# Optimization experiments

Hardware: AMD Instinct MI355X
Metric: run time of the kernel (lower is better)

The kernel has to match this reference:

```python
import jax, jax.numpy as jnp
import numpy as np

D_MODEL = 1024
NUM_HEADS = 16
HEAD_DIM = D_MODEL // NUM_HEADS
THETA = 10000.0


def _rope(x):
    # x: [B, H, S, Dk]; interleaved even/odd rotation as in the torch module
    *_, seq_len, d_k = x.shape
    d = d_k // 2
    inv_freq = 1.0 / (THETA ** (2.0 * jnp.arange(d, dtype=jnp.float32) / d_k))
    pos = jnp.arange(seq_len, dtype=jnp.float32)
    angles = pos[:, None] * inv_freq[None, :]  # [S, d]
    cos = jnp.cos(angles)
    sin = jnp.sin(angles)
    x_even = x[..., 0::2]
    x_odd = x[..., 1::2]
    rot_even = x_even * cos - x_odd * sin
    rot_odd = x_even * sin + x_odd * cos
    return jnp.stack([rot_even, rot_odd], axis=-1).reshape(x.shape)


def setup_inputs() -> dict:
    key = jax.random.key(0)
    ks = jax.random.split(key, 5)
    B, S = 4, 2048
    x = jax.random.normal(ks[0], (B, S, D_MODEL), dtype=jnp.float32)
    q_w = jax.random.uniform(ks[1], (D_MODEL, D_MODEL), dtype=jnp.float32)
    k_w = jax.random.uniform(ks[2], (D_MODEL, D_MODEL), dtype=jnp.float32)
    v_w = jax.random.uniform(ks[3], (D_MODEL, D_MODEL), dtype=jnp.float32)
    o_w = jax.random.uniform(ks[4], (D_MODEL, D_MODEL), dtype=jnp.float32)
    return {"x": x, "q_w": q_w, "k_w": k_w, "v_w": v_w, "o_w": o_w}


def reference(x, q_w, k_w, v_w, o_w):
    B, S, _ = x.shape
    def split_heads(t):
        return t.reshape(B, S, NUM_HEADS, HEAD_DIM).transpose(0, 2, 1, 3)  # [B,H,S,Dk]
    Q = split_heads(x @ q_w.T)
    K = split_heads(x @ k_w.T)
    V = split_heads(x @ v_w.T)
    Q = _rope(Q)
    K = _rope(K)
    scale = 1.0 / jnp.sqrt(jnp.float32(HEAD_DIM))
    scores = jnp.einsum('bhqd,bhkd->bhqk', Q, K) * scale  # [B,H,S,S]
    causal = jnp.tril(jnp.ones((S, S), dtype=bool))
    scores = jnp.where(causal[None, None], scores, -jnp.inf)
    attn = jax.nn.softmax(scores, axis=-1)
    out = jnp.einsum('bhqk,bhkd->bhqd', attn, V)  # [B,H,S,Dk]
    out = out.transpose(0, 2, 1, 3).reshape(B, S, D_MODEL)
    return out @ o_w.T
```

## Files before the change

### kernel.cpp

```cpp
#include <hip/hip_runtime.h>
#include <hip/hip_bf16.h>
#include <cstdint>
#include <cstddef>

#define D_MODEL   1024
#define NUM_HEADS 16
#define HEAD_DIM  64
#define SEQ       2048
#define BATCH     4
#define BH        (BATCH*NUM_HEADS)
#define MROWS     (BATCH*SEQ)

typedef _Float16 half8  __attribute__((ext_vector_type(8)));
typedef _Float16 half4v __attribute__((ext_vector_type(4)));
typedef float    floatx4 __attribute__((ext_vector_type(4)));

__device__ inline void gld_lds16(const void* g, void* l) {
    __builtin_amdgcn_global_load_lds(
        (__attribute__((address_space(1))) void*)g,
        (__attribute__((address_space(3))) void*)l,
        16, 0, 0);
}

__global__ void rope_table(float2* __restrict__ tab) {
    const int i = blockIdx.x * blockDim.x + threadIdx.x;
    const int p = i & 31, s = i >> 5;
    const double inv = pow(10000.0, -(double)p / 32.0);
    const double ang = (double)s * inv;
    tab[i] = make_float2((float)cos(ang), (float)sin(ang));
}

__global__ void f32_split_f16(const float* __restrict__ in,
                              _Float16* __restrict__ hi,
                              _Float16* __restrict__ lo, int n4) {
    int i = blockIdx.x * blockDim.x + threadIdx.x;
    if (i >= n4) return;
    float4 v = ((const float4*)in)[i];
    half4v h = { (_Float16)v.x, (_Float16)v.y, (_Float16)v.z, (_Float16)v.w };
    half4v l = { (_Float16)(v.x - (float)h.x), (_Float16)(v.y - (float)h.y),
                 (_Float16)(v.z - (float)h.z), (_Float16)(v.w - (float)h.w) };
    ((half4v*)hi)[i] = h;
    ((half4v*)lo)[i] = l;
}

__global__ void conv_weights(const float* __restrict__ qw, const float* __restrict__ kw,
                             const float* __restrict__ vw, const float* __restrict__ ow,
                             _Float16* __restrict__ qwh, _Float16* __restrict__ qwl,
                             _Float16* __restrict__ kwh, _Float16* __restrict__ kwl,
                             _Float16* __restrict__ vwh, _Float16* __restrict__ owh) {
    const int i = blockIdx.x * blockDim.x + threadIdx.x;
    const int which = i >> 18;
    const int j = i & 262143;
    const float4 v = ((const float4*)(which == 0 ? qw : which == 1 ? kw :
                                      which == 2 ? vw : ow))[j];
    half4v h = { (_Float16)v.x, (_Float16)v.y, (_Float16)v.z, (_Float16)v.w };
    if (which < 2) {
        half4v l = { (_Float16)(v.x - (float)h.x), (_Float16)(v.y - (float)h.y),
                     (_Float16)(v.z - (float)h.z), (_Float16)(v.w - (float)h.w) };
        ((half4v*)(which ? kwh : qwh))[j] = h;
        ((half4v*)(which ? kwl : qwl))[j] = l;
    } else {
        ((half4v*)(which == 2 ? vwh : owh))[j] = h;
    }
}

__global__ __launch_bounds__(256)
void gemm_bt(const _Float16* __restrict__ A, const _Float16* __restrict__ B,
             float* __restrict__ Cout, int M, int N, int K) {
    __shared__ _Float16 As[128*32];
    __shared__ _Float16 Bs[128*32];

    const int nb = N >> 7;
    const int bx = blockIdx.x % nb;
    const int by = blockIdx.x / nb;
    const int m0 = by << 7, n0 = bx << 7;

    const int t    = threadIdx.x;
    const int w    = t >> 6;
    const int lane = t & 63;
    const int r    = lane & 15;
    const int quad = lane >> 4;
    const int wm   = (w >> 1) << 6;
    const int wn   = (w & 1) << 6;

    const int srow = lane >> 2;
    const int scol = (lane & 3) << 3;

    floatx4 acc[4][4];
    #pragma unroll
    for (int i = 0; i < 4; i++)
        #pragma unroll
        for (int j = 0; j < 4; j++)
            acc[i][j] = (floatx4){0.f, 0.f, 0.f, 0.f};

    for (int k0 = 0; k0 < K; k0 += 32) {
        __syncthreads();
        #pragma unroll
        for (int p = 0; p < 2; ++p) {
            const int rbase = p*64 + w*16;
            gld_lds16(&A[(size_t)(m0 + rbase + srow)*K + k0 + scol], &As[rbase*32]);
            gld_lds16(&B[(size_t)(n0 + rbase + srow)*K + k0 + scol], &Bs[rbase*32]);
        }
        __syncthreads();

        half8 af[4], bf[4];
        #pragma unroll
        for (int i = 0; i < 4; i++)
            af[i] = *(const half8*)&As[(wm + i*16 + r)*32 + quad*8];
        #pragma unroll
        for (int j = 0; j < 4; j++)
            bf[j] = *(const half8*)&Bs[(wn + j*16 + r)*32 + quad*8];

        #pragma unroll
        for (int i = 0; i < 4; i++)
            #pragma unroll
            for (int j = 0; j < 4; j++)
                acc[i][j] = __builtin_amdgcn_mfma_f32_16x16x32_f16(
                                af[i], bf[j], acc[i][j], 0, 0, 0);
    }

    #pragma unroll
    for (int i = 0; i < 4; i++)
        #pragma unroll
        for (int j = 0; j < 4; j++)
            #pragma unroll
            for (int v = 0; v < 4; v++) {
                const int m = m0 + wm + i*16 + quad*4 + v;
                const int n = n0 + wn + j*16 + r;
                Cout[(size_t)m*N + n] = acc[i][j][v];
            }
}

__global__ __launch_bounds__(256)
void gemm_qkv(const _Float16* __restrict__ Axh, const _Float16* __restrict__ Axl,
              const _Float16* __restrict__ qwh, const _Float16* __restrict__ qwl,
              const _Float16* __restrict__ kwh, const _Float16* __restrict__ kwl,
              const _Float16* __restrict__ vwh,
              _Float16* __restrict__ Qhi, _Float16* __restrict__ Qlo,
              _Float16* __restrict__ Khi, _Float16* __restrict__ Klo,
              _Float16* __restrict__ Vt,  const float2* __restrict__ tab) {
    __shared__ _Float16 smem[4*4096];
    _Float16* Ash = smem;
    _Float16* Asl = smem + 4096;
    _Float16* Bsh = smem + 8192;
    _Float16* Bsl = smem + 12288;

    const int bxa = blockIdx.x;
    const int bx  = bxa % 24;
    const int by  = bxa / 24;
    const int wt  = bx >> 3;
    const int n0  = (bx & 7) << 7;
    const int m0  = by << 7;

    const _Float16* Bh = (wt == 0) ? qwh : (wt == 1) ? kwh : vwh;
    const _Float16* Bl = (wt == 0) ? qwl : kwl;

    const int t    = threadIdx.x;
    const int w    = t >> 6;
    const int lane = t & 63;
    const int r    = lane & 15;
    const int quad = lane >> 4;
    const int wm   = (w >> 1) << 6;
    const int wn   = (w & 1) << 6;

    const int srow = lane >> 2;
    const int scol = (lane & 3) << 3;

    floatx4 acc[4][4];
    #pragma unroll
    for (int i = 0; i < 4; i++)
        #pragma unroll
        for (int j = 0; j < 4; j++)
            acc[i][j] = (floatx4){0.f, 0.f, 0.f, 0.f};

    for (int k0 = 0; k0 < 1024; k0 += 32) {
        __syncthreads();
        #pragma unroll
        for (int p = 0; p < 2; ++p) {
            const int rbase = p*64 + w*16;
            const size_t ga = (size_t)(m0 + rbase + srow)*1024 + k0 + scol;
            const size_t gb = (size_t)(n0 + rbase + srow)*1024 + k0 + scol;
            gld_lds16(&Axh[ga], &Ash[rbase*32]);
            gld_lds16(&Bh [gb], &Bsh[rbase*32]);
            if (wt < 2) {
                gld_lds16(&Axl[ga], &Asl[rbase*32]);
                gld_lds16(&Bl [gb], &Bsl[rbase*32]);
            }
        }
        __syncthreads();

        half8 ah[4], bh[4];
        #pragma unroll
        for (int i = 0; i < 4; i++)
            ah[i] = *(const half8*)&Ash[(wm + i*16 + r)*32 + quad*8];
        #pragma unroll
        for (int j = 0; j < 4; j++)
            bh[j] = *(const half8*)&Bsh[(wn + j*16 + r)*32 + quad*8];

        if (wt < 2) {
            half8 al[4], bl[4];
            #pragma unroll
            for (int i = 0; i < 4; i++)
                al[i] = *(const half8*)&Asl[(wm + i*16 + r)*32 + quad*8];
            #pragma unroll
            for (int j = 0; j < 4; j++)
                bl[j] = *(const half8*)&Bsl[(wn + j*16 + r)*32 + quad*8];
            #pragma unroll
            for (int i = 0; i < 4; i++)
                #pragma unroll
                for (int j = 0; j < 4; j++) {
                    acc[i][j] = __builtin_amdgcn_mfma_f32_16x16x32_f16(
                                    ah[i], bh[j], acc[i][j], 0, 0, 0);
                    acc[i][j] = __builtin_amdgcn_mfma_f32_16x16x32_f16(
                                    ah[i], bl[j], acc[i][j], 0, 0, 0);
                    acc[i][j] = __builtin_amdgcn_mfma_f32_16x16x32_f16(
                                    al[i], bh[j], acc[i][j], 0, 0, 0);
                }
        } else {
            #pragma unroll
            for (int i = 0; i < 4; i++)
                #pragma unroll
                for (int j = 0; j < 4; j++)
                    acc[i][j] = __builtin_amdgcn_mfma_f32_16x16x32_f16(
                                    ah[i], bh[j], acc[i][j], 0, 0, 0);
        }
    }

    __syncthreads();
    float* sc = (float*)smem + w*1088;
    const int g  = lane & 7;
    const int rw = lane >> 3;
    const int hh = (n0 + wn) >> 6;

    if (wt < 2) {
        _Float16* Chi = wt ? Khi : Qhi;
        _Float16* Clo = wt ? Klo : Qlo;
        #pragma unroll
        for (int i = 0; i < 4; i++) {
            #pragma unroll
            for (int j = 0; j < 4; j++)
                #pragma unroll
                for (int v = 0; v < 4; v++)
                    sc[(quad*4 + v)*68 + j*16 + r] = acc[i][j][v];
            #pragma unroll
            for (int rg = 0; rg < 2; rg++) {
                const int row = rw + rg*8;
                const int m   = m0 + wm + i*16 + row;
                const int bb  = m >> 11, s_ = m & 2047;
                const float4 va = *(const float4*)&sc[row*68 + g*8];
                const float4 vb = *(const float4*)&sc[row*68 + g*8 + 4];
                const float vv[8] = {va.x, va.y, va.z, va.w,
                                     vb.x, vb.y, vb.z, vb.w};
                half8 hv, lv;
                #pragma unroll
                for (int p2 = 0; p2 < 4; p2++) {
                    const float2 cs = tab[s_*32 + g*4 + p2];
                    const float e0 = vv[2*p2], o0 = vv[2*p2+1];
                    const float re = e0*cs.x - o0*cs.y;
                    const float ro = e0*cs.y + o0*cs.x;
                    const _Float16 rh = (_Float16)re;
                    const _Float16 oh = (_Float16)ro;
                    hv[2*p2]   = rh; lv[2*p2]   = (_Float16)(re - (float)rh);
                    hv[2*p2+1] = oh; lv[2*p2+1] = (_Float16)(ro - (float)oh);
                }
                const size_t idx = ((((size_t)bb*NUM_HEADS + hh)*SEQ + s_) << 6) + g*8;
                *(half8*)&Chi[idx] = hv;
                *(half8*)&Clo[idx] = lv;
            }
        }
    } else {
        const int d = lane;
        #pragma unroll
        for (int i = 0; i < 4; i++) {
            #pragma unroll
            for (int j = 0; j < 4; j++)
                #pragma unroll
                for (int v = 0; v < 4; v++)
                    sc[(quad*4 + v)*68 + j*16 + r] = acc[i][j][v];
            #pragma unroll
            for (int rg = 0; rg < 2; rg++) {
                const int m  = m0 + wm + i*16 + rg*8;
                const int bb = m >> 11, s_ = m & 2047;
                half8 ov;
                #pragma unroll
                for (int rr = 0; rr < 8; rr++)
                    ov[rr] = (_Float16)sc[(rg*8 + rr)*68 + d];
                *(half8*)&Vt[((((size_t)bb*NUM_HEADS + hh)*HEAD_DIM + d) << 11) + s_] = ov;
            }
        }
    }
}

#define PSTR 72
__global__ __launch_bounds__(256)
void flash_attn(const _Float16* __restrict__ Qhi, const _Float16* __restrict__ Qlo,
                const _Float16* __restrict__ Khi, const _Float16* __restrict__ Klo,
                const _Float16* __restrict__ Vt,  _Float16* __restrict__ AO) {
    __shared__ _Float16 SB[2][6][64*32];
    __shared__ _Float16 Pl[4][16*PSTR];

    const int t    = threadIdx.x;
    const int w    = t >> 6;
    const int lane = t & 63;
    const int r    = lane & 15;
    const int quad = lane >> 4;

    const int bx = blockIdx.x;
    const int bh = bx & 63;
    const int qb = 31 - (bx >> 6);
    const int q0w = qb*64 + w*16;
    const int b  = bh >> 4, h = bh & 15;

    const _Float16* Qh_ = Qhi + (size_t)bh * SEQ * HEAD_DIM;
    const _Float16* Ql_ = Qlo + (size_t)bh * SEQ * HEAD_DIM;
    const _Float16* Khg = Khi + (size_t)bh * SEQ * HEAD_DIM;
    const _Float16* Klg = Klo + (size_t)bh * SEQ * HEAD_DIM;
    const _Float16* Vtg = Vt  + (size_t)bh * HEAD_DIM * SEQ;

    half8 qh[2], ql[2];
    #pragma unroll
    for (int c = 0; c < 2; ++c) {
        qh[c] = *(const half8*)&Qh_[(size_t)(q0w + r)*64 + c*32 + quad*8];
        ql[c] = *(const half8*)&Ql_[(size_t)(q0w + r)*64 + c*32 + quad*8];
    }

    floatx4 ot[4];
    #pragma unroll
    for (int dt = 0; dt < 4; ++dt) ot[dt] = (floatx4){0.f,0.f,0.f,0.f};
    float mi = -1e30f, li = 0.f;

    const int sr = lane >> 2;
    const int sc = (lane & 3) << 3;
    const int rb = w << 4;

    auto stage = [&](int buf, int kt) {
        const int k0  = kt << 6;
        const int row = rb + sr;
        const size_t kr = (size_t)(k0 + row)*64;
        gld_lds16(&Khg[kr +      sc], &SB[buf][0][rb*32]);
        gld_lds16(&Khg[kr + 32 + sc], &SB[buf][1][rb*32]);
        gld_lds16(&Klg[kr +      sc], &SB[buf][2][rb*32]);
        gld_lds16(&Klg[kr + 32 + sc], &SB[buf][3][rb*32]);
        const size_t vr = (size_t)row*SEQ + k0;
        gld_lds16(&Vtg[vr +      sc], &SB[buf][4][rb*32]);
        gld_lds16(&Vtg[vr + 32 + sc], &SB[buf][5][rb*32]);
    };

    const int niter = qb + 1;
    stage(0, 0);
    int cur = 0;

    for (int kt = 0; kt < niter; ++kt) {
        const int k0 = kt << 6;

        __syncthreads();
        if (kt + 1 < niter) stage(cur ^ 1, kt + 1);

        const _Float16* Kh0 = SB[cur][0];
        const _Float16* Kh1 = SB[cur][1];
        const _Float16* Kl0 = SB[cur][2];
        const _Float16* Kl1 = SB[cur][3];
        const _Float16* Vp0 = SB[cur][4];
        const _Float16* Vp1 = SB[cur][5];

        float s[16];
        __builtin_amdgcn_s_setprio(1);
        #pragma unroll
        for (int sub = 0; sub < 4; ++sub) {
            floatx4 a = (floatx4){0.f,0.f,0.f,0.f};
            const int fr = (sub*16 + r)*32 + quad*8;
            const half8 kh0 = *(const half8*)&Kh0[fr];
            const half8 kh1 = *(const half8*)&Kh1[fr];
            const half8 kl0 = *(const half8*)&Kl0[fr];
            const half8 kl1 = *(const half8*)&Kl1[fr];
            a = __builtin_amdgcn_mfma_f32_16x16x32_f16(kh0, qh[0], a, 0, 0, 0);
            a = __builtin_amdgcn_mfma_f32_16x16x32_f16(kh1, qh[1], a, 0, 0, 0);
            a = __builtin_amdgcn_mfma_f32_16x16x32_f16(kh0, ql[0], a, 0, 0, 0);
            a = __builtin_amdgcn_mfma_f32_16x16x32_f16(kh1, ql[1], a, 0, 0, 0);
            a = __builtin_amdgcn_mfma_f32_16x16x32_f16(kl0, qh[0], a, 0, 0, 0);
            a = __builtin_amdgcn_mfma_f32_16x16x32_f16(kl1, qh[1], a, 0, 0, 0);
            #pragma unroll
            for (int v = 0; v < 4; ++v) s[sub*4 + v] = a[v] * 0.125f;
        }
        __builtin_amdgcn_s_setprio(0);

        if (kt == niter - 1) {
            #pragma unroll
            for (int sub = 0; sub < 4; ++sub)
                #pragma unroll
                for (int v = 0; v < 4; ++v)
                    if (k0 + sub*16 + quad*4 + v > q0w + r)
                        s[sub*4 + v] = -1e30f;
        }

        float tm = s[0];
        #pragma unroll
        for (int i = 1; i < 16; ++i) tm = fmaxf(tm, s[i]);
        tm = fmaxf(tm, __shfl_xor(tm, 16));
        tm = fmaxf(tm, __shfl_xor(tm, 32));
        const float mn = fmaxf(mi, tm);
        const float alpha = __expf(mi - mn);
        mi = mn;
        float rs = 0.f;
        #pragma unroll
        for (int i = 0; i < 16; ++i) { s[i] = __expf(s[i] - mn); rs += s[i]; }
        rs += __shfl_xor(rs, 16);
        rs += __shfl_xor(rs, 32);
        li = li*alpha + rs;
        #pragma unroll
        for (int dt = 0; dt < 4; ++dt)
            #pragma unroll
            for (int v = 0; v < 4; ++v) ot[dt][v] *= alpha;

        #pragma unroll
        for (int sub = 0; sub < 4; ++sub) {
            half4v pk = { (_Float16)s[sub*4+0], (_Float16)s[sub*4+1],
                          (_Float16)s[sub*4+2], (_Float16)s[sub*4+3] };
            *(half4v*)&Pl[w][r*PSTR + sub*16 + quad*4] = pk;
        }

        __builtin_amdgcn_s_setprio(1);
        #pragma unroll
        for (int c = 0; c < 2; ++c) {
            const half8 pf = *(const half8*)&Pl[w][r*PSTR + c*32 + quad*8];
            const _Float16* Vsc = c ? Vp1 : Vp0;
            #pragma unroll
            for (int dt = 0; dt < 4; ++dt) {
                const half8 vf = *(const half8*)&Vsc[(dt*16 + r)*32 + quad*8];
                ot[dt] = __builtin_amdgcn_mfma_f32_16x16x32_f16(vf, pf, ot[dt], 0, 0, 0);
            }
        }
        __builtin_amdgcn_s_setprio(0);

        cur ^= 1;
    }

    const float inv = 1.0f / li;
    const int q = q0w + r;
    #pragma unroll
    for (int dt = 0; dt < 4; ++dt) {
        half4v o = { (_Float16)(ot[dt][0]*inv), (_Float16)(ot[dt][1]*inv),
                     (_Float16)(ot[dt][2]*inv), (_Float16)(ot[dt][3]*inv) };
        *(half4v*)&AO[((size_t)(b*SEQ + q))*D_MODEL + h*HEAD_DIM + dt*16 + quad*4] = o;
    }
}

extern "C" void kernel_launch(void* const* d_in, const int* in_sizes, int n_in,
                              void* d_out, int out_size, void* d_ws, size_t ws_size,
                              hipStream_t stream) {
    const float* x  = (const float*)d_in[0];
    const float* qw = (const float*)d_in[1];
    const float* kw = (const float*)d_in[2];
    const float* vw = (const float*)d_in[3];
    const float* ow = (const float*)d_in[4];
    float* out = (float*)d_out;

    _Float16* xh  = (_Float16*)d_ws;
    _Float16* xl  = xh  + (size_t)MROWS * D_MODEL;
    _Float16* qwh = xl  + (size_t)MROWS * D_MODEL;
    _Float16* qwl = qwh + (size_t)D_MODEL * D_MODEL;
    _Float16* kwh = qwl + (size_t)D_MODEL * D_MODEL;
    _Float16* kwl = kwh + (size_t)D_MODEL * D_MODEL;
    _Float16* vwh = kwl + (size_t)D_MODEL * D_MODEL;
    _Float16* owh = vwh + (size_t)D_MODEL * D_MODEL;
    _Float16* Qhi = owh + (size_t)D_MODEL * D_MODEL;
    _Float16* Qlo = Qhi + (size_t)MROWS * D_MODEL;
    _Float16* Khi = Qlo + (size_t)MROWS * D_MODEL;
    _Float16* Klo = Khi + (size_t)MROWS * D_MODEL;
    _Float16* Vt  = Klo + (size_t)MROWS * D_MODEL;
    _Float16* AO  = Vt  + (size_t)MROWS * D_MODEL;
    float2*   tab = (float2*)(AO + (size_t)MROWS * D_MODEL);

    rope_table<<<(SEQ*32)/256, 256, 0, stream>>>(tab);

    const int nx4 = MROWS * D_MODEL / 4;
    f32_split_f16<<<nx4/256, 256, 0, stream>>>(x, xh, xl, nx4);
    conv_weights<<<(4*262144)/256, 256, 0, stream>>>(qw, kw, vw, ow,
                                                     qwh, qwl, kwh, kwl, vwh, owh);

    gemm_qkv<<<64*24, 256, 0, stream>>>(xh, xl, qwh, qwl, kwh, kwl, vwh,
                                        Qhi, Qlo, Khi, Klo, Vt, tab);

    flash_attn<<<BH * (SEQ/64), 256, 0, stream>>>(Qhi, Qlo, Khi, Klo, Vt, AO);

    gemm_bt<<<(MROWS/128)*(D_MODEL/128), 256, 0, stream>>>(AO, owh, out,
                                                           MROWS, D_MODEL, D_MODEL);
}
```

Measured before the change: 389.3 us.

## Process two 64-row query groups per flash-attention block to reuse K/V tiles

Each flash-attention block now covers 128 query rows, split into two 64-row groups, instead of 64. Every wave keeps two independent online-softmax states and applies each staged K/V tile to both groups, which halves the number of K/V tile loads per query row. The price is more registers, half as many blocks (1024), and a longer critical path per block.

```diff
diff --git a/kernel.cpp b/kernel.cpp
--- a/kernel.cpp
+++ b/kernel.cpp
@@ -307,8 +307,10 @@
 
     const int bx = blockIdx.x;
     const int bh = bx & 63;
-    const int qb = 31 - (bx >> 6);
-    const int q0w = qb*64 + w*16;
+    const int qb = 15 - (bx >> 6);
+    const int Q0 = qb << 7;
+    const int q0a = Q0 + w*16;
+    const int q0b = Q0 + 64 + w*16;
     const int b  = bh >> 4, h = bh & 15;
 
     const _Float16* Qh_ = Qhi + (size_t)bh * SEQ * HEAD_DIM;
@@ -317,17 +319,22 @@
     const _Float16* Klg = Klo + (size_t)bh * SEQ * HEAD_DIM;
     const _Float16* Vtg = Vt  + (size_t)bh * HEAD_DIM * SEQ;
 
-    half8 qh[2], ql[2];
+    half8 qh0[2], ql0[2], qh1[2], ql1[2];
     #pragma unroll
     for (int c = 0; c < 2; ++c) {
-        qh[c] = *(const half8*)&Qh_[(size_t)(q0w + r)*64 + c*32 + quad*8];
-        ql[c] = *(const half8*)&Ql_[(size_t)(q0w + r)*64 + c*32 + quad*8];
-    }
-
-    floatx4 ot[4];
+        qh0[c] = *(const half8*)&Qh_[(size_t)(q0a + r)*64 + c*32 + quad*8];
+        ql0[c] = *(const half8*)&Ql_[(size_t)(q0a + r)*64 + c*32 + quad*8];
+        qh1[c] = *(const half8*)&Qh_[(size_t)(q0b + r)*64 + c*32 + quad*8];
+        ql1[c] = *(const half8*)&Ql_[(size_t)(q0b + r)*64 + c*32 + quad*8];
+    }
+
+    floatx4 ot0[4], ot1[4];
     #pragma unroll
-    for (int dt = 0; dt < 4; ++dt) ot[dt] = (floatx4){0.f,0.f,0.f,0.f};
-    float mi = -1e30f, li = 0.f;
+    for (int dt = 0; dt < 4; ++dt) {
+        ot0[dt] = (floatx4){0.f,0.f,0.f,0.f};
+        ot1[dt] = (floatx4){0.f,0.f,0.f,0.f};
+    }
+    float mi0 = -1e30f, li0 = 0.f, mi1 = -1e30f, li1 = 0.f;
 
     const int sr = lane >> 2;
     const int sc = (lane & 3) << 3;
@@ -346,7 +353,7 @@
         gld_lds16(&Vtg[vr + 32 + sc], &SB[buf][5][rb*32]);
     };
 
-    const int niter = qb + 1;
+    const int niter = 2*qb + 2;
     stage(0, 0);
     int cur = 0;
 
@@ -363,85 +370,103 @@
         const _Float16* Vp0 = SB[cur][4];
         const _Float16* Vp1 = SB[cur][5];
 
-        float s[16];
-        __builtin_amdgcn_s_setprio(1);
-        #pragma unroll
-        for (int sub = 0; sub < 4; ++sub) {
-            floatx4 a = (floatx4){0.f,0.f,0.f,0.f};
-            const int fr = (sub*16 + r)*32 + quad*8;
-            const half8 kh0 = *(const half8*)&Kh0[fr];
-            const half8 kh1 = *(const half8*)&Kh1[fr];
-            const half8 kl0 = *(const half8*)&Kl0[fr];
-            const half8 kl1 = *(const half8*)&Kl1[fr];
-            a = __builtin_amdgcn_mfma_f32_16x16x32_f16(kh0, qh[0], a, 0, 0, 0);
-            a = __builtin_amdgcn_mfma_f32_16x16x32_f16(kh1, qh[1], a, 0, 0, 0);
-            a = __builtin_amdgcn_mfma_f32_16x16x32_f16(kh0, ql[0], a, 0, 0, 0);
-            a = __builtin_amdgcn_mfma_f32_16x16x32_f16(kh1, ql[1], a, 0, 0, 0);
-            a = __builtin_amdgcn_mfma_f32_16x16x32_f16(kl0, qh[0], a, 0, 0, 0);
-            a = __builtin_amdgcn_mfma_f32_16x16x32_f16(kl1, qh[1], a, 0, 0, 0);
-            #pragma unroll
-            for (int v = 0; v < 4; ++v) s[sub*4 + v] = a[v] * 0.125f;
-        }
-        __builtin_amdgcn_s_setprio(0);
-
-        if (kt == niter - 1) {
-            #pragma unroll
-            for (int sub = 0; sub < 4; ++sub)
-                #pragma unroll
-                for (int v = 0; v < 4; ++v)
-                    if (k0 + sub*16 + quad*4 + v > q0w + r)
-                        s[sub*4 + v] = -1e30f;
-        }
-
-        float tm = s[0];
-        #pragma unroll
-        for (int i = 1; i < 16; ++i) tm = fmaxf(tm, s[i]);
-        tm = fmaxf(tm, __shfl_xor(tm, 16));
-        tm = fmaxf(tm, __shfl_xor(tm, 32));
-        const float mn = fmaxf(mi, tm);
-        const float alpha = __expf(mi - mn);
-        mi = mn;
-        float rs = 0.f;
-        #pragma unroll
-        for (int i = 0; i < 16; ++i) { s[i] = __expf(s[i] - mn); rs += s[i]; }
-        rs += __shfl_xor(rs, 16);
-        rs += __shfl_xor(rs, 32);
-        li = li*alpha + rs;
-        #pragma unroll
-        for (int dt = 0; dt < 4; ++dt)
-            #pragma unroll
-            for (int v = 0; v < 4; ++v) ot[dt][v] *= alpha;
-
-        #pragma unroll
-        for (int sub = 0; sub < 4; ++sub) {
-            half4v pk = { (_Float16)s[sub*4+0], (_Float16)s[sub*4+1],
-                          (_Float16)s[sub*4+2], (_Float16)s[sub*4+3] };
-            *(half4v*)&Pl[w][r*PSTR + sub*16 + quad*4] = pk;
-        }
-
-        __builtin_amdgcn_s_setprio(1);
-        #pragma unroll
-        for (int c = 0; c < 2; ++c) {
-            const half8 pf = *(const half8*)&Pl[w][r*PSTR + c*32 + quad*8];
-            const _Float16* Vsc = c ? Vp1 : Vp0;
-            #pragma unroll
-            for (int dt = 0; dt < 4; ++dt) {
-                const half8 vf = *(const half8*)&Vsc[(dt*16 + r)*32 + quad*8];
-                ot[dt] = __builtin_amdgcn_mfma_f32_16x16x32_f16(vf, pf, ot[dt], 0, 0, 0);
-            }
-        }
-        __builtin_amdgcn_s_setprio(0);
+        auto group = [&](int q0g, const half8 (&qhg)[2], const half8 (&qlg)[2],
+                         floatx4 (&og)[4], float &mig, float &lig, bool domask) {
+            float s[16];
+            __builtin_amdgcn_s_setprio(1);
+            #pragma unroll
+            for (int sub = 0; sub < 4; ++sub) {
+                floatx4 a = (floatx4){0.f,0.f,0.f,0.f};
+                const int fr = (sub*16 + r)*32 + quad*8;
+                const half8 kh0 = *(const half8*)&Kh0[fr];
+                const half8 kh1 = *(const half8*)&Kh1[fr];
+                const half8 kl0 = *(const half8*)&Kl0[fr];
+                const half8 kl1 = *(const half8*)&Kl1[fr];
+                a = __builtin_amdgcn_mfma_f32_16x16x32_f16(kh0, qhg[0], a, 0, 0, 0);
+                a = __builtin_amdgcn_mfma_f32_16x16x32_f16(kh1, qhg[1], a, 0, 0, 0);
+                a = __builtin_amdgcn_mfma_f32_16x16x32_f16(kh0, qlg[0], a, 0, 0, 0);
+                a = __builtin_amdgcn_mfma_f32_16x16x32_f16(kh1, qlg[1], a, 0, 0, 0);
+                a = __builtin_amdgcn_mfma_f32_16x16x32_f16(kl0, qhg[0], a, 0, 0, 0);
+                a = __builtin_amdgcn_mfma_f32_16x16x32_f16(kl1, qhg[1], a, 0, 0, 0);
+                #pragma unroll
+                for (int v = 0; v < 4; ++v) s[sub*4 + v] = a[v] * 0.125f;
+            }
+            __builtin_amdgcn_s_setprio(0);
+
+            if (domask) {
+                #pragma unroll
+                for (int sub = 0; sub < 4; ++sub)
+                    #pragma unroll
+                    for (int v = 0; v < 4; ++v)
+                        if (k0 + sub*16 + quad*4 + v > q0g + r)
+                            s[sub*4 + v] = -1e30f;
+            }
+
+            float tm = s[0];
+            #pragma unroll
+            for (int i = 1; i < 16; ++i) tm = fmaxf(tm, s[i]);
+            tm = fmaxf(tm, __shfl_xor(tm, 16));
+            tm = fmaxf(tm, __shfl_xor(tm, 32));
+            const float mn = fmaxf(mig, tm);
+            const float alpha = __expf(mig - mn);
+            mig = mn;
+            float rs = 0.f;
+            #pragma unroll
+            for (int i = 0; i < 16; ++i) { s[i] = __expf(s[i] - mn); rs += s[i]; }
+            rs += __shfl_xor(rs, 16);
+            rs += __shfl_xor(rs, 32);
+            lig = lig*alpha + rs;
+            #pragma unroll
+            for (int dt = 0; dt < 4; ++dt)
+                #pragma unroll
+                for (int v = 0; v < 4; ++v) og[dt][v] *= alpha;
+
+            #pragma unroll
+            for (int sub = 0; sub < 4; ++sub) {
+                half4v pk = { (_Float16)s[sub*4+0], (_Float16)s[sub*4+1],
+                              (_Float16)s[sub*4+2], (_Float16)s[sub*4+3] };
+                *(half4v*)&Pl[w][r*PSTR + sub*16 + quad*4] = pk;
+            }
+
+            __builtin_amdgcn_s_setprio(1);
+            #pragma unroll
+            for (int c = 0; c < 2; ++c) {
+                const half8 pf = *(const half8*)&Pl[w][r*PSTR + c*32 + quad*8];
+                const _Float16* Vsc = c ? Vp1 : Vp0;
+                #pragma unroll
+                for (int dt = 0; dt < 4; ++dt) {
+                    const half8 vf = *(const half8*)&Vsc[(dt*16 + r)*32 + quad*8];
+                    og[dt] = __builtin_amdgcn_mfma_f32_16x16x32_f16(vf, pf, og[dt], 0, 0, 0);
+                }
+            }
+            __builtin_amdgcn_s_setprio(0);
+        };
+
+        if (kt <= 2*qb) group(q0a, qh0, ql0, ot0, mi0, li0, kt == 2*qb);
+        group(q0b, qh1, ql1, ot1, mi1, li1, kt == 2*qb + 1);
 
         cur ^= 1;
     }
 
-    const float inv = 1.0f / li;
-    const int q = q0w + r;
-    #pragma unroll
-    for (int dt = 0; dt < 4; ++dt) {
-        half4v o = { (_Float16)(ot[dt][0]*inv), (_Float16)(ot[dt][1]*inv),
-                     (_Float16)(ot[dt][2]*inv), (_Float16)(ot[dt][3]*inv) };
-        *(half4v*)&AO[((size_t)(b*SEQ + q))*D_MODEL + h*HEAD_DIM + dt*16 + quad*4] = o;
+    {
+        const float inv0 = 1.0f / li0;
+        const int q = q0a + r;
+        #pragma unroll
+        for (int dt = 0; dt < 4; ++dt) {
+            half4v o = { (_Float16)(ot0[dt][0]*inv0), (_Float16)(ot0[dt][1]*inv0),
+                         (_Float16)(ot0[dt][2]*inv0), (_Float16)(ot0[dt][3]*inv0) };
+            *(half4v*)&AO[((size_t)(b*SEQ + q))*D_MODEL + h*HEAD_DIM + dt*16 + quad*4] = o;
+        }
+    }
+    {
+        const float inv1 = 1.0f / li1;
+        const int q = q0b + r;
+        #pragma unroll
+        for (int dt = 0; dt < 4; ++dt) {
+            half4v o = { (_Float16)(ot1[dt][0]*inv1), (_Float16)(ot1[dt][1]*inv1),
+                         (_Float16)(ot1[dt][2]*inv1), (_Float16)(ot1[dt][3]*inv1) };
+            *(half4v*)&AO[((size_t)(b*SEQ + q))*D_MODEL + h*HEAD_DIM + dt*16 + quad*4] = o;
+        }
     }
 }
 
@@ -481,7 +506,7 @@
     gemm_qkv<<<64*24, 256, 0, stream>>>(xh, xl, qwh, qwl, kwh, kwl, vwh,
                                         Qhi, Qlo, Khi, Klo, Vt, tab);
 
-    flash_attn<<<BH * (SEQ/64), 256, 0, stream>>>(Qhi, Qlo, Khi, Klo, Vt, AO);
+    flash_attn<<<BH * (SEQ/128), 256, 0, stream>>>(Qhi, Qlo, Khi, Klo, Vt, AO);
 
     gemm_bt<<<(MROWS/128)*(D_MODEL/128), 256, 0, stream>>>(AO, owh, out,
                                                            MROWS, D_MODEL, D_MODEL);
```

New measurement: 384.8 us. About the same (-1.2%).
